# Kernel optimization log

Measured on AMD Instinct MI355X. Metric: run time of the kernel, lower is better.

The kernel has to match this reference:

```python
import jax, jax.numpy as jnp
import numpy as np

V, E, H, L = 37, 256, 512, 3
B, S = 512, 128


def lstm_layer(x, W_ih, W_hh, b_ih, b_hh):
    # x: [B,S,D_in]; W_ih: [4H,D_in]; W_hh: [4H,H]; PyTorch gate order i,f,g,o
    Bx = x.shape[0]
    Hh = W_hh.shape[1]
    x_proj = jnp.einsum('bsd,gd->bsg', x, W_ih) + b_ih + b_hh  # [B,S,4H]

    def step(carry, xt):
        h, c = carry
        gates = xt + h @ W_hh.T
        i, f, g, o = jnp.split(gates, 4, axis=-1)
        i = jax.nn.sigmoid(i)
        f = jax.nn.sigmoid(f)
        g = jnp.tanh(g)
        o = jax.nn.sigmoid(o)
        c = f * c + i * g
        h = o * jnp.tanh(c)
        return (h, c), h

    init = (jnp.zeros((Bx, Hh), x.dtype), jnp.zeros((Bx, Hh), x.dtype))
    (hT, cT), hs = jax.lax.scan(step, init, jnp.swapaxes(x_proj, 0, 1))
    return jnp.swapaxes(hs, 0, 1), hT, cT


def setup_inputs() -> dict:
    key = jax.random.key(0)
    ks = jax.random.split(key, 16)
    inp = {'tokens': jax.random.randint(ks[0], (B, S), 0, V)}
    inp['embedding'] = jax.random.normal(ks[1], (V, E), jnp.float32) * 0.05
    for l in range(L):
        d_in = E if l == 0 else H
        inp[f'W_ih{l}'] = jax.random.normal(ks[2 + 4 * l], (4 * H, d_in), jnp.float32) * 0.05
        inp[f'W_hh{l}'] = jax.random.normal(ks[3 + 4 * l], (4 * H, H), jnp.float32) * 0.05
        inp[f'b_ih{l}'] = jnp.zeros((4 * H,), jnp.float32)
        inp[f'b_hh{l}'] = jnp.zeros((4 * H,), jnp.float32)
    inp['W_out'] = jax.random.normal(ks[14], (V, H), jnp.float32) * 0.05
    inp['b_out'] = jnp.zeros((V,), jnp.float32)
    return inp


def reference(tokens, embedding, W_ih0, W_hh0, b_ih0, b_hh0,
              W_ih1, W_hh1, b_ih1, b_hh1,
              W_ih2, W_hh2, b_ih2, b_hh2, W_out, b_out):
    x = embedding[tokens]  # [B,S,E]
    hs, cs = [], []
    for (Wi, Wh, bi, bh) in ((W_ih0, W_hh0, b_ih0, b_hh0),
                             (W_ih1, W_hh1, b_ih1, b_hh1),
                             (W_ih2, W_hh2, b_ih2, b_hh2)):
        x, hT, cT = lstm_layer(x, Wi, Wh, bi, bh)
        hs.append(hT)
        cs.append(cT)
    logits = jnp.einsum('bsh,vh->bsv', x, W_out) + b_out  # [B,S,V]
    return logits, jnp.stack(hs), jnp.stack(cs)
```

## Files before the change

kernel.cpp:

```cpp
#include <hip/hip_runtime.h>

typedef __attribute__((ext_vector_type(4))) float f32x4;
typedef __attribute__((ext_vector_type(8))) short bf16x8;

#define DEV __device__ __forceinline__

DEV float b2f(ushort u) { return __uint_as_float(((uint)u) << 16); }
DEV ushort f2b(float f) {
    uint u = __float_as_uint(f);
    return (ushort)((u + 0x7fffu + ((u >> 16) & 1u)) >> 16);
}
DEV float fsig(float x) {
    return __builtin_amdgcn_rcpf(1.f + __builtin_amdgcn_exp2f(-1.4426950408889634f * x));
}
DEV float ftanh(float x) {
    return 1.f - 2.f * __builtin_amdgcn_rcpf(__builtin_amdgcn_exp2f(2.885390081777927f * x) + 1.f);
}
DEV void gload_lds16(const void* g, void* l) {
    __builtin_amdgcn_global_load_lds(
        (const __attribute__((address_space(1))) void*)g,
        (__attribute__((address_space(3))) void*)l, 16, 0, 0);
}
DEV void gload_lds16_l2(const void* g, void* l) {
    __builtin_amdgcn_global_load_lds(
        (const __attribute__((address_space(1))) void*)g,
        (__attribute__((address_space(3))) void*)l, 16, 0, 1);
}
DEV void store_sc_u32(uint* p, uint v) {
    asm volatile("global_store_dword %0, %1, off sc0 sc1" :: "v"(p), "v"(v) : "memory");
}
DEV uint load_sc_u32(const uint* p) {
    uint v;
    asm volatile("global_load_dword %0, %1, off sc0 sc1\n\ts_waitcnt vmcnt(0)"
                 : "=v"(v) : "v"(p) : "memory");
    return v;
}

__global__ void f2b_kernel(const float* __restrict__ s, ushort* __restrict__ d, int n) {
    int i = blockIdx.x * 256 + threadIdx.x;
    if (i < n) d[i] = f2b(s[i]);
}

__global__ void embed_kernel(const int* __restrict__ tok, const float* __restrict__ emb,
                             ushort* __restrict__ x0) {
    int row = blockIdx.x;
    int t = row >> 9, b = row & 511;
    int tk = tok[b * 128 + t];
    x0[(size_t)row * 256 + threadIdx.x] = f2b(emb[(size_t)tk * 256 + threadIdx.x]);
}

__global__ __launch_bounds__(256) void gemm_bias_kernel(
    const ushort* __restrict__ A, const ushort* __restrict__ Bw,
    const float* __restrict__ bias0, const float* __restrict__ bias1,
    ushort* __restrict__ C, int M, int N, int K) {
    __shared__ ushort la[128 * 32];
    __shared__ ushort lb[128 * 32];
    const int tid = threadIdx.x;
    const int wave = tid >> 6, lane = tid & 63;
    const int ntn = N >> 7;
    const int tm = blockIdx.x / ntn, tn = blockIdx.x % ntn;
    const int m0 = tm << 7, n0 = tn << 7;
    const int wm = (wave >> 1) * 64, wn = (wave & 1) * 64;
    f32x4 acc[4][4] = {};
    const int nks = K >> 5;
    const int srow = tid >> 2, scol = (tid & 3) * 8;
    for (int ks = 0; ks < nks; ++ks) {
        const int k0 = ks << 5;
#pragma unroll
        for (int r = 0; r < 2; ++r) {
            gload_lds16(A + (size_t)(m0 + r * 64 + srow) * K + k0 + scol, &la[r * 2048 + wave * 512]);
            gload_lds16(Bw + (size_t)(n0 + r * 64 + srow) * K + k0 + scol, &lb[r * 2048 + wave * 512]);
        }
        __syncthreads();
        bf16x8 af[4], bfr[4];
#pragma unroll
        for (int i = 0; i < 4; ++i)
            af[i] = *(const bf16x8*)&la[(wm + i * 16 + (lane & 15)) * 32 + (lane >> 4) * 8];
#pragma unroll
        for (int i = 0; i < 4; ++i)
            bfr[i] = *(const bf16x8*)&lb[(wn + i * 16 + (lane & 15)) * 32 + (lane >> 4) * 8];
#pragma unroll
        for (int mi = 0; mi < 4; ++mi)
#pragma unroll
            for (int ni = 0; ni < 4; ++ni)
                acc[mi][ni] = __builtin_amdgcn_mfma_f32_16x16x32_bf16(af[mi], bfr[ni], acc[mi][ni], 0, 0, 0);
        __syncthreads();
    }
#pragma unroll
    for (int mi = 0; mi < 4; ++mi) {
        int row = m0 + wm + mi * 16 + ((lane >> 4) << 2);
#pragma unroll
        for (int j = 0; j < 4; ++j) {
#pragma unroll
            for (int ni = 0; ni < 4; ++ni) {
                int col = n0 + wn + ni * 16 + (lane & 15);
                C[(size_t)(row + j) * N + col] = f2b(acc[mi][ni][j] + bias0[col] + bias1[col]);
            }
        }
    }
}

__global__ __launch_bounds__(256) void lstm_chunk_kernel(
    const ushort* __restrict__ xpj,
    const ushort* __restrict__ Whh,
    ushort* __restrict__ hs,
    float* __restrict__ cstate,
    float* __restrict__ hT, float* __restrict__ cT,
    uint* __restrict__ bar,
    int t0) {
    __shared__ ushort hp[64 * 512];
    __shared__ float gbuf[4][64][20];
    const int tid = threadIdx.x;
    const int wave = tid >> 6, lane = tid & 63;
    const int grp = blockIdx.x & 7;
    const int hsl = blockIdx.x >> 3;
    const int b0 = grp << 6, h0 = hsl << 4;
    uint* gflags = bar + grp * 512;
    uint* myflag = gflags + hsl * 16;

    __threadfence();

    bf16x8 Bfr[16];
    const ushort* wb = Whh + ((size_t)(wave * 512 + h0 + (lane & 15))) * 512 + (lane >> 4) * 8;
#pragma unroll
    for (int ks = 0; ks < 16; ++ks) Bfr[ks] = *(const bf16x8*)(wb + ks * 32);

    float creg[4];
#pragma unroll
    for (int i = 0; i < 2; ++i) {
        const int e2 = i * 512 + tid * 2;
        const size_t ci = (size_t)(b0 + (e2 >> 4)) * 512 + h0 + (e2 & 15);
        if (t0 > 0) {
            float2 cv = *(const float2*)&cstate[ci];
            creg[2 * i] = cv.x; creg[2 * i + 1] = cv.y;
        } else {
            creg[2 * i] = 0.f; creg[2 * i + 1] = 0.f;
        }
    }

    for (int tt = 0; tt < 32; ++tt) {
        const int t = t0 + tt;
        uint xq[2][4];
        const ushort* xt = xpj + (size_t)tt * 1048576;
#pragma unroll
        for (int i = 0; i < 2; ++i) {
            const int e2 = i * 512 + tid * 2;
            const uint* xb = (const uint*)(xt + (size_t)(b0 + (e2 >> 4)) * 2048 + h0 + (e2 & 15));
            xq[i][0] = xb[0]; xq[i][1] = xb[256]; xq[i][2] = xb[512]; xq[i][3] = xb[768];
        }
        if (tt > 0) {
            if (wave == 0) {
                const uint* fp = gflags + ((lane & 31) << 4);
                const uint target = (uint)tt;
                while (!__all(load_sc_u32(fp) >= target)) __builtin_amdgcn_s_sleep(1);
            }
            __syncthreads();
        }
        f32x4 acc[4] = {};
        if (t > 0) {
            const ushort* hprev = hs + (size_t)(t - 1) * 262144;
#pragma unroll
            for (int rr = 0; rr < 16; ++rr) {
                const int row = rr * 4 + wave;
                gload_lds16_l2(hprev + (size_t)(b0 + row) * 512 + ((lane ^ (row & 7)) * 8),
                               &hp[row * 512]);
            }
            __syncthreads();
#pragma unroll
            for (int ks = 0; ks < 16; ++ks) {
#pragma unroll
                for (int mi = 0; mi < 4; ++mi) {
                    const int row = mi * 16 + (lane & 15);
                    const int c16 = (ks * 4 + (lane >> 4)) ^ (row & 7);
                    bf16x8 af = *(const bf16x8*)&hp[row * 512 + c16 * 8];
                    acc[mi] = __builtin_amdgcn_mfma_f32_16x16x32_bf16(af, Bfr[ks], acc[mi], 0, 0, 0);
                }
            }
        }
#pragma unroll
        for (int mi = 0; mi < 4; ++mi) {
            const int rloc = mi * 16 + ((lane >> 4) << 2);
#pragma unroll
            for (int j = 0; j < 4; ++j) gbuf[wave][rloc + j][lane & 15] = acc[mi][j];
        }
        __syncthreads();
        ushort* hout = hs + (size_t)t * 262144;
#pragma unroll
        for (int i = 0; i < 2; ++i) {
            const int e2 = i * 512 + tid * 2;
            const int b = e2 >> 4, hh = e2 & 15;
            float2 gI = *(const float2*)&gbuf[0][b][hh];
            float2 gF = *(const float2*)&gbuf[1][b][hh];
            float2 gG = *(const float2*)&gbuf[2][b][hh];
            float2 gO = *(const float2*)&gbuf[3][b][hh];
            float i0 = fsig(gI.x + b2f((ushort)(xq[i][0] & 0xffff)));
            float i1 = fsig(gI.y + b2f((ushort)(xq[i][0] >> 16)));
            float f0 = fsig(gF.x + b2f((ushort)(xq[i][1] & 0xffff)));
            float f1 = fsig(gF.y + b2f((ushort)(xq[i][1] >> 16)));
            float g0 = ftanh(gG.x + b2f((ushort)(xq[i][2] & 0xffff)));
            float g1 = ftanh(gG.y + b2f((ushort)(xq[i][2] >> 16)));
            float o0 = fsig(gO.x + b2f((ushort)(xq[i][3] & 0xffff)));
            float o1 = fsig(gO.y + b2f((ushort)(xq[i][3] >> 16)));
            float c0 = f0 * creg[2 * i] + i0 * g0;
            float c1 = f1 * creg[2 * i + 1] + i1 * g1;
            float h0v = o0 * ftanh(c0);
            float h1v = o1 * ftanh(c1);
            creg[2 * i] = c0; creg[2 * i + 1] = c1;
            const size_t ci = (size_t)(b0 + b) * 512 + h0 + hh;
            store_sc_u32((uint*)(hout + ci), (uint)f2b(h0v) | ((uint)f2b(h1v) << 16));
            if (t == 127) {
                *(float2*)&hT[ci] = make_float2(h0v, h1v);
                *(float2*)&cT[ci] = make_float2(c0, c1);
            }
        }
        if (tt < 31) {
            asm volatile("s_waitcnt vmcnt(0)" ::: "memory");
            __syncthreads();
            if (tid == 0) store_sc_u32(myflag, (uint)(tt + 1));
        }
    }
#pragma unroll
    for (int i = 0; i < 2; ++i) {
        const int e2 = i * 512 + tid * 2;
        const size_t ci = (size_t)(b0 + (e2 >> 4)) * 512 + h0 + (e2 & 15);
        *(float2*)&cstate[ci] = make_float2(creg[2 * i], creg[2 * i + 1]);
    }
}

__global__ __launch_bounds__(256) void outproj_kernel(
    const ushort* __restrict__ hs, const float* __restrict__ Wout,
    const float* __restrict__ bout, float* __restrict__ out) {
    __shared__ ushort lh[32 * 512];
    const int tid = threadIdx.x;
    const size_t r0 = (size_t)blockIdx.x * 32;
    const uint4* gs = (const uint4*)(hs + r0 * 512);
    uint4* ls = (uint4*)lh;
    for (int i = tid; i < 2048; i += 256) ls[i] = gs[i];
    __syncthreads();
    const int rg = tid & 7, vg = tid >> 3;
    float acc[4][2] = {};
    for (int k8 = 0; k8 < 64; ++k8) {
        float hf[4][8];
#pragma unroll
        for (int rr = 0; rr < 4; ++rr) {
            bf16x8 hv = *(const bf16x8*)&lh[(rg * 4 + rr) * 512 + k8 * 8];
#pragma unroll
            for (int j = 0; j < 8; ++j) hf[rr][j] = b2f((ushort)hv[j]);
        }
#pragma unroll
        for (int vi = 0; vi < 2; ++vi) {
            int v = vg + vi * 32;
            if (v < 37) {
                const float* wp = Wout + (size_t)v * 512 + k8 * 8;
                float4 w0 = *(const float4*)wp;
                float4 w1 = *(const float4*)(wp + 4);
                float wv[8] = {w0.x, w0.y, w0.z, w0.w, w1.x, w1.y, w1.z, w1.w};
#pragma unroll
                for (int rr = 0; rr < 4; ++rr) {
                    float s = 0.f;
#pragma unroll
                    for (int j = 0; j < 8; ++j) s += hf[rr][j] * wv[j];
                    acc[rr][vi] += s;
                }
            }
        }
    }
#pragma unroll
    for (int vi = 0; vi < 2; ++vi) {
        int v = vg + vi * 32;
        if (v < 37) {
#pragma unroll
            for (int rr = 0; rr < 4; ++rr) {
                size_t r = r0 + rg * 4 + rr;
                int t = (int)(r >> 9), b = (int)(r & 511);
                out[((size_t)b * 128 + t) * 37 + v] = acc[rr][vi] + bout[v];
            }
        }
    }
}

extern "C" void kernel_launch(void* const* d_in, const int* in_sizes, int n_in,
                              void* d_out, int out_size, void* d_ws, size_t ws_size,
                              hipStream_t stream) {
    (void)in_sizes; (void)n_in; (void)out_size; (void)ws_size;
    const int* tokens = (const int*)d_in[0];
    const float* emb = (const float*)d_in[1];
    const float* Wih_f[3] = {(const float*)d_in[2], (const float*)d_in[6], (const float*)d_in[10]};
    const float* Whh_f[3] = {(const float*)d_in[3], (const float*)d_in[7], (const float*)d_in[11]};
    const float* bih[3] = {(const float*)d_in[4], (const float*)d_in[8], (const float*)d_in[12]};
    const float* bhh[3] = {(const float*)d_in[5], (const float*)d_in[9], (const float*)d_in[13]};
    const float* Wout = (const float*)d_in[14];
    const float* bout = (const float*)d_in[15];
    float* out = (float*)d_out;

    char* ws = (char*)d_ws;
    size_t off = 0;
    auto take = [&](size_t nb) -> void* {
        void* p = ws + off;
        off = (off + nb + 255) & ~(size_t)255;
        return p;
    };
    ushort* x0 = (ushort*)take((size_t)128 * 512 * 256 * 2);
    ushort* hsA = (ushort*)take((size_t)128 * 512 * 512 * 2);
    ushort* hsB = (ushort*)take((size_t)128 * 512 * 512 * 2);
    ushort* xpj = (ushort*)take((size_t)32 * 512 * 2048 * 2);
    float* cst = (float*)take((size_t)512 * 512 * 4);
    ushort* wih[3];
    wih[0] = (ushort*)take((size_t)2048 * 256 * 2);
    wih[1] = (ushort*)take((size_t)2048 * 512 * 2);
    wih[2] = (ushort*)take((size_t)2048 * 512 * 2);
    ushort* whh[3];
    for (int l = 0; l < 3; ++l) whh[l] = (ushort*)take((size_t)2048 * 512 * 2);
    uint* barbase = (uint*)take((size_t)12 * 4096 * 4);

    hipMemsetAsync(barbase, 0, (size_t)12 * 4096 * 4, stream);

    f2b_kernel<<<2048, 256, 0, stream>>>(Wih_f[0], wih[0], 2048 * 256);
    f2b_kernel<<<4096, 256, 0, stream>>>(Wih_f[1], wih[1], 2048 * 512);
    f2b_kernel<<<4096, 256, 0, stream>>>(Wih_f[2], wih[2], 2048 * 512);
    for (int l = 0; l < 3; ++l)
        f2b_kernel<<<4096, 256, 0, stream>>>(Whh_f[l], whh[l], 2048 * 512);

    embed_kernel<<<65536, 256, 0, stream>>>(tokens, emb, x0);

    float* hTbase = out + 2424832;
    float* cTbase = out + 2424832 + 786432;
    const ushort* src = x0;
    ushort* hs_out = hsA;
    for (int l = 0; l < 3; ++l) {
        int K = (l == 0) ? 256 : 512;
        hs_out = (l == 1) ? hsB : hsA;
        for (int ch = 0; ch < 4; ++ch) {
            gemm_bias_kernel<<<2048, 256, 0, stream>>>(
                src + (size_t)ch * 16384 * K, wih[l], bih[l], bhh[l], xpj, 16384, 2048, K);
            lstm_chunk_kernel<<<256, 256, 0, stream>>>(
                xpj, whh[l], hs_out, cst,
                hTbase + (size_t)l * 262144, cTbase + (size_t)l * 262144,
                barbase + (size_t)(l * 4 + ch) * 4096, ch * 32);
        }
        src = hs_out;
    }
    outproj_kernel<<<2048, 256, 0, stream>>>(hs_out, Wout, bout, out);
}
```

Measured before the change: 2.517 ms.

## Retile recurrent MFMA as 2x2 wave grid with fragment-ordered LDS layout

Each wave now computes a 2x2 block of 16x16 tiles (two batch tiles times two gate groups) instead of one gate group across all four batch tiles. LDS A-operand reads drop from four per k-step to two, since each A fragment is reused across two weight fragments. The h tile is now stored in LDS in MFMA-fragment order (one contiguous 1KB chunk per k-step and batch tile), so lanes read consecutive 16-byte vectors with no XOR swizzle. In exchange each wave holds twice as many W_hh fragments in registers (32 bf16x8), which raises VGPR pressure and could lower occupancy.

```diff
diff --git a/kernel.cpp b/kernel.cpp
--- a/kernel.cpp
+++ b/kernel.cpp
@@ -109,9 +109,11 @@
     uint* __restrict__ bar,
     int t0) {
     __shared__ ushort hp[64 * 512];
-    __shared__ float gbuf[4][64][20];
+    __shared__ float gbuf[4][64][18];
     const int tid = threadIdx.x;
-    const int wave = tid >> 6, lane = tid & 63;
+    const int w = tid >> 6, lane = tid & 63;
+    const int l15 = lane & 15, lh = lane >> 4;
+    const int wr = w >> 1, wc = w & 1;
     const int grp = blockIdx.x & 7;
     const int hsl = blockIdx.x >> 3;
     const int b0 = grp << 6, h0 = hsl << 4;
@@ -120,10 +122,13 @@
 
     __threadfence();
 
-    bf16x8 Bfr[16];
-    const ushort* wb = Whh + ((size_t)(wave * 512 + h0 + (lane & 15))) * 512 + (lane >> 4) * 8;
-#pragma unroll
-    for (int ks = 0; ks < 16; ++ks) Bfr[ks] = *(const bf16x8*)(wb + ks * 32);
+    bf16x8 Bfr[2][16];
+#pragma unroll
+    for (int gg = 0; gg < 2; ++gg) {
+        const ushort* wb = Whh + (size_t)((2 * wc + gg) * 512 + h0 + l15) * 512 + lh * 8;
+#pragma unroll
+        for (int ks = 0; ks < 16; ++ks) Bfr[gg][ks] = *(const bf16x8*)(wb + ks * 32);
+    }
 
     float creg[4];
 #pragma unroll
@@ -149,40 +154,41 @@
             xq[i][0] = xb[0]; xq[i][1] = xb[256]; xq[i][2] = xb[512]; xq[i][3] = xb[768];
         }
         if (tt > 0) {
-            if (wave == 0) {
+            if (w == 0) {
                 const uint* fp = gflags + ((lane & 31) << 4);
                 const uint target = (uint)tt;
                 while (!__all(load_sc_u32(fp) >= target)) __builtin_amdgcn_s_sleep(1);
             }
             __syncthreads();
         }
-        f32x4 acc[4] = {};
+        f32x4 acc[2][2] = {};
         if (t > 0) {
             const ushort* hprev = hs + (size_t)(t - 1) * 262144;
 #pragma unroll
-            for (int rr = 0; rr < 16; ++rr) {
-                const int row = rr * 4 + wave;
-                gload_lds16_l2(hprev + (size_t)(b0 + row) * 512 + ((lane ^ (row & 7)) * 8),
-                               &hp[row * 512]);
+            for (int i = 0; i < 16; ++i) {
+                const int c = i * 4 + w;
+                const int ks = c >> 2, mi = c & 3;
+                gload_lds16_l2(hprev + (size_t)(b0 + mi * 16 + l15) * 512 + ks * 32 + lh * 8,
+                               &hp[c * 512]);
             }
             __syncthreads();
 #pragma unroll
             for (int ks = 0; ks < 16; ++ks) {
-#pragma unroll
-                for (int mi = 0; mi < 4; ++mi) {
-                    const int row = mi * 16 + (lane & 15);
-                    const int c16 = (ks * 4 + (lane >> 4)) ^ (row & 7);
-                    bf16x8 af = *(const bf16x8*)&hp[row * 512 + c16 * 8];
-                    acc[mi] = __builtin_amdgcn_mfma_f32_16x16x32_bf16(af, Bfr[ks], acc[mi], 0, 0, 0);
-                }
-            }
-        }
-#pragma unroll
-        for (int mi = 0; mi < 4; ++mi) {
-            const int rloc = mi * 16 + ((lane >> 4) << 2);
-#pragma unroll
-            for (int j = 0; j < 4; ++j) gbuf[wave][rloc + j][lane & 15] = acc[mi][j];
-        }
+                bf16x8 A0 = *(const bf16x8*)&hp[(ks * 4 + 2 * wr) * 512 + lane * 8];
+                bf16x8 A1 = *(const bf16x8*)&hp[(ks * 4 + 2 * wr + 1) * 512 + lane * 8];
+                acc[0][0] = __builtin_amdgcn_mfma_f32_16x16x32_bf16(A0, Bfr[0][ks], acc[0][0], 0, 0, 0);
+                acc[0][1] = __builtin_amdgcn_mfma_f32_16x16x32_bf16(A0, Bfr[1][ks], acc[0][1], 0, 0, 0);
+                acc[1][0] = __builtin_amdgcn_mfma_f32_16x16x32_bf16(A1, Bfr[0][ks], acc[1][0], 0, 0, 0);
+                acc[1][1] = __builtin_amdgcn_mfma_f32_16x16x32_bf16(A1, Bfr[1][ks], acc[1][1], 0, 0, 0);
+            }
+        }
+#pragma unroll
+        for (int m = 0; m < 2; ++m)
+#pragma unroll
+            for (int gg = 0; gg < 2; ++gg)
+#pragma unroll
+                for (int j = 0; j < 4; ++j)
+                    gbuf[2 * wc + gg][(2 * wr + m) * 16 + lh * 4 + j][l15] = acc[m][gg][j];
         __syncthreads();
         ushort* hout = hs + (size_t)t * 262144;
 #pragma unroll
```

Result: slower. 2.903 ms (+15.3%).
